# Optimization experiments

Hardware: AMD Instinct MI355X
Metric: run time of the kernel (lower is better)

Reference implementation:

```python
import jax, jax.numpy as jnp
import numpy as np

B = 16384          # batch
IN = 256           # input_dim
HID = [1024, 1024, 512]
K = 8              # num_mixtures
D = 16             # latent_dim
NT = D * (D + 1) // 2  # 136 packed tril components per mixture

_rows, _cols = np.tril_indices(D)          # row-major lower-tri order, same as nested loops
_rows = jnp.asarray(_rows); _cols = jnp.asarray(_cols)
_diag_mask = _rows == _cols                # [NT] bool


def setup_inputs() -> dict:
    key = jax.random.key(0)
    ks = jax.random.split(key, 12)

    def lin(k, fi, fo):
        kw, kb = jax.random.split(k)
        s = 1.0 / np.sqrt(fi)
        W = (jax.random.uniform(kw, (fi, fo), minval=-s, maxval=s)).astype(jnp.float32)
        b = (jax.random.uniform(kb, (fo,), minval=-s, maxval=s)).astype(jnp.float32)
        return W, b

    W0, b0 = lin(ks[0], IN, HID[0])
    W1, b1 = lin(ks[1], HID[0], HID[1])
    W2, b2 = lin(ks[2], HID[1], HID[2])
    Wpi, bpi = lin(ks[3], HID[2], K)
    Wmu, bmu = lin(ks[4], HID[2], K * D)
    Wt, bt = lin(ks[5], HID[2], K * NT)
    x = jax.random.normal(ks[6], (B, IN), dtype=jnp.float32)
    return dict(x=x, W0=W0, b0=b0, W1=W1, b1=b1, W2=W2, b2=b2,
                Wpi=Wpi, bpi=bpi, Wmu=Wmu, bmu=bmu, Wt=Wt, bt=bt)


def reference(x, W0, b0, W1, b1, W2, b2, Wpi, bpi, Wmu, bmu, Wt, bt):
    # MLP trunk: Linear + ReLU chain
    h = jax.nn.relu(x @ W0 + b0)
    h = jax.nn.relu(h @ W1 + b1)
    h = jax.nn.relu(h @ W2 + b2)
    # Heads
    pi_k = jax.nn.softmax(h @ Wpi + bpi, axis=1)                 # [B, K]
    mu_k = (h @ Wmu + bmu).reshape(-1, K, D)                     # [B, K, D]
    tc = (h @ Wt + bt).reshape(-1, K, NT)                        # [B, K, NT]
    # Fused cholesky-tril assembly: exp on diagonal entries, copy off-diagonal,
    # scattered into lower triangle in row-major (i, j<=i) order.
    vals = jnp.where(_diag_mask, jnp.exp(tc), tc)                # [B, K, NT]
    tril = jnp.zeros((tc.shape[0], K, D, D), dtype=tc.dtype)
    tril = tril.at[:, :, _rows, _cols].set(vals)                 # [B, K, D, D]
    return pi_k, mu_k, tril
```

## Files before the change

### kernel.cpp

```cpp
#include <hip/hip_runtime.h>
#include <hip/hip_bf16.h>
#include <cstdint>
#include <cstddef>

typedef __attribute__((ext_vector_type(8))) _Float16 half8;
typedef __attribute__((ext_vector_type(4))) float f32x4;
typedef __attribute__((ext_vector_type(8))) unsigned short ushort8v;
typedef __attribute__((ext_vector_type(4))) unsigned short ushort4v;

__device__ __forceinline__ unsigned short f2h_bits(float x) {
  _Float16 h = (_Float16)x;
  union { _Float16 h; unsigned short u; } cv; cv.h = h; return cv.u;
}

__device__ __forceinline__ void barrier_raw() {
  asm volatile("" ::: "memory");
  __builtin_amdgcn_s_barrier();
  asm volatile("" ::: "memory");
}
__device__ __forceinline__ void lgkm0() {
  asm volatile("s_waitcnt lgkmcnt(0)" ::: "memory");
}
template<int N> __device__ __forceinline__ void vmw() {
  static_assert(N == 0 || N == 3 || N == 4, "unsupported vmcnt");
  if constexpr (N == 0) asm volatile("s_waitcnt vmcnt(0)" ::: "memory");
  if constexpr (N == 3) asm volatile("s_waitcnt vmcnt(3)" ::: "memory");
  if constexpr (N == 4) asm volatile("s_waitcnt vmcnt(4)" ::: "memory");
}


__global__ __launch_bounds__(256) void k_f32_to_f16(const float* __restrict__ src,
                                                    unsigned short* __restrict__ dst, int n4) {
  int i = blockIdx.x * 256 + threadIdx.x;
  if (i >= n4) return;
  float4 v = ((const float4*)src)[i];
  ushort4v o;
  o[0] = f2h_bits(v.x); o[1] = f2h_bits(v.y); o[2] = f2h_bits(v.z); o[3] = f2h_bits(v.w);
  ((ushort4v*)dst)[i] = o;
}

__global__ __launch_bounds__(256) void k_transpose_f16(const float* __restrict__ W,
                                                       unsigned short* __restrict__ Wt,
                                                       int Kd, int N) {
  int tid = blockIdx.x * 256 + threadIdx.x;
  int total = (Kd >> 3) * N;
  if (tid >= total) return;
  int kc = tid / N;
  int n  = tid - kc * N;
  int k0 = kc << 3;
  ushort8v o;
#pragma unroll
  for (int j = 0; j < 8; ++j) o[j] = f2h_bits(W[(size_t)(k0 + j) * N + n]);
  *(ushort8v*)(&Wt[(size_t)n * Kd + k0]) = o;
}

__global__ __launch_bounds__(256) void k_build_head(
    const float* __restrict__ Wmu, const float* __restrict__ Wt,
    const float* __restrict__ Wpi,
    const float* __restrict__ bmu, const float* __restrict__ bt,
    const float* __restrict__ bpi,
    unsigned short* __restrict__ whd, float* __restrict__ bhd)
{
  int tid = blockIdx.x * 256 + threadIdx.x;
  if (tid >= 2304 * 64) return;
  int r  = tid >> 6;
  int d0 = (tid & 63) << 3;

  const float* src = nullptr; int stride = 0;
  if (r < 128) { src = Wmu + r; stride = 128; }
  else if (r < 2176) {
    int rU = r - 128, k = rU >> 8, i = (rU >> 4) & 15, j = rU & 15;
    if (j <= i) { src = Wt + k * 136 + ((i * (i + 1)) >> 1) + j; stride = 1088; }
  } else if (r < 2184) { src = Wpi + (r - 2176); stride = 8; }

  ushort8v o;
#pragma unroll
  for (int jj = 0; jj < 8; ++jj)
    o[jj] = src ? f2h_bits(src[(size_t)(d0 + jj) * stride]) : (unsigned short)0;
  *(ushort8v*)(&whd[(size_t)r * 512 + d0]) = o;

  if (d0 == 0) {
    float b = 0.f;
    if (r < 128) b = bmu[r];
    else if (r < 2176) {
      int rU = r - 128, k = rU >> 8, i = (rU >> 4) & 15, j = rU & 15;
      if (j <= i) b = bt[k * 136 + ((i * (i + 1)) >> 1) + j];
    } else if (r < 2184) b = bpi[r - 2176];
    bhd[r] = b;
  }
}


__device__ __forceinline__ void epi_relu_h(const f32x4& a, const float* bias, int col0,
                                           unsigned short* Hout, size_t row, int N) {
  float4 b4 = *(const float4*)&bias[col0];
  ushort4v o;
  float v0 = a[0] + b4.x; o[0] = f2h_bits(v0 > 0.f ? v0 : 0.f);
  float v1 = a[1] + b4.y; o[1] = f2h_bits(v1 > 0.f ? v1 : 0.f);
  float v2 = a[2] + b4.z; o[2] = f2h_bits(v2 > 0.f ? v2 : 0.f);
  float v3 = a[3] + b4.w; o[3] = f2h_bits(v3 > 0.f ? v3 : 0.f);
  *(ushort4v*)&Hout[row * N + col0] = o;
}

__device__ __forceinline__ void epi_head(const f32x4& a, const float* bias, int col0,
                                         size_t row, float* out_pi, float* out_mu,
                                         float* out_tril) {
  if (col0 >= 2184) return;
  float4 b4 = *(const float4*)&bias[col0];
  float v[4] = { a[0] + b4.x, a[1] + b4.y, a[2] + b4.z, a[3] + b4.w };
  if (col0 < 128) {
    *(float4*)&out_mu[row * 128 + col0] = make_float4(v[0], v[1], v[2], v[3]);
  } else if (col0 < 2176) {
    const int cc0 = col0 - 128;
    const int i   = (cc0 >> 4) & 15;
    const int j0  = cc0 & 15;
#pragma unroll
    for (int r = 0; r < 4; ++r) if (j0 + r == i) v[r] = expf(v[r]);
    *(float4*)&out_tril[row * 2048 + cc0] = make_float4(v[0], v[1], v[2], v[3]);
  } else {
    float m4 = fmaxf(fmaxf(v[0], v[1]), fmaxf(v[2], v[3]));
    float mx = fmaxf(m4, __shfl_xor(m4, 16));
    float e[4], s4 = 0.f;
#pragma unroll
    for (int r = 0; r < 4; ++r) { e[r] = expf(v[r] - mx); s4 += e[r]; }
    float sm = s4 + __shfl_xor(s4, 16);
    *(float4*)&out_pi[row * 8 + (col0 - 2176)] =
        make_float4(e[0] / sm, e[1] / sm, e[2] / sm, e[3] / sm);
  }
}


template<int EPI>
__global__ __launch_bounds__(256) void k_gemm2p(
    const unsigned short* __restrict__ A,
    const unsigned short* __restrict__ Bt,
    int Kd, int N, int nNb,
    const float* __restrict__ bias,
    unsigned short* __restrict__ Hout,
    float* __restrict__ out_pi,
    float* __restrict__ out_mu,
    float* __restrict__ out_tril)
{
  __shared__ unsigned short Alds[2][128 * 32];
  __shared__ unsigned short Blds[2][128 * 32];

  const int tid  = threadIdx.x;
  const int lane = tid & 63;
  const int wv   = tid >> 6;
  const int wr   = wv >> 1;
  const int wc   = wv & 1;
  const int l15  = lane & 15;
  const int lk   = lane >> 4;

  const int cpx = gridDim.x >> 3;
  const int bid = blockIdx.x;
  const int swz = (bid & 7) * cpx + (bid >> 3);
  const int bm  = (swz / nNb) << 7;
  const int bn  = (swz % nNb) << 7;

  f32x4 acc[4][4] = {};

  const int srow = lane >> 2;
  const int scol = (lane & 3) << 3;

  const unsigned short* aBase = A  + (size_t)bm * Kd;
  const unsigned short* bBase = Bt + (size_t)bn * Kd;

  auto stage = [&](int bb, int k0) {
#pragma unroll
    for (int c = 0; c < 2; ++c) {
      const int chunk = (wv << 1) + c;
      const int row = (chunk << 4) + srow;
      __builtin_amdgcn_global_load_lds(
          (const __attribute__((address_space(1))) void*)(aBase + (size_t)row * Kd + k0 + scol),
          (__attribute__((address_space(3))) void*)(&Alds[bb][chunk << 9]),
          16, 0, 0);
      __builtin_amdgcn_global_load_lds(
          (const __attribute__((address_space(1))) void*)(bBase + (size_t)row * Kd + k0 + scol),
          (__attribute__((address_space(3))) void*)(&Blds[bb][chunk << 9]),
          16, 0, 0);
    }
  };

  const int nk = Kd >> 5;
  stage(0, 0);
  __syncthreads();
  int cur = 0;
  for (int kt = 0; kt < nk; ++kt) {
    if (kt + 1 < nk) stage(cur ^ 1, (kt + 1) << 5);

    const unsigned short* al = &Alds[cur][((wr << 6) + l15) * 32 + (lk << 3)];
    const unsigned short* bl = &Blds[cur][((wc << 6) + l15) * 32 + (lk << 3)];
    half8 af[4], bfr[4];
#pragma unroll
    for (int m = 0; m < 4; ++m) af[m]  = *(const half8*)(al + (m << 9));
#pragma unroll
    for (int n = 0; n < 4; ++n) bfr[n] = *(const half8*)(bl + (n << 9));
#pragma unroll
    for (int m = 0; m < 4; ++m)
#pragma unroll
      for (int n = 0; n < 4; ++n)
        acc[m][n] = __builtin_amdgcn_mfma_f32_16x16x32_f16(bfr[n], af[m], acc[m][n], 0, 0, 0);

    __syncthreads();
    cur ^= 1;
  }

#pragma unroll
  for (int m = 0; m < 4; ++m) {
    const size_t row = bm + (wr << 6) + (m << 4) + l15;
#pragma unroll
    for (int n = 0; n < 4; ++n) {
      const int col0 = bn + (wc << 6) + (n << 4) + (lk << 2);
      if (EPI == 0) epi_relu_h(acc[m][n], bias, col0, Hout, row, N);
      else          epi_head(acc[m][n], bias, col0, row, out_pi, out_mu, out_tril);
    }
  }
}


template<int NH, int M_rep>
__device__ __forceinline__ void mfma_phase(const half8* af, const half8* bf,
                                           f32x4 (*acc)[4]) {
  __builtin_amdgcn_s_setprio(1);
#pragma unroll
  for (int m = 0; m < M_rep; ++m) {
    acc[m][NH * 2 + 0] = __builtin_amdgcn_mfma_f32_16x16x32_f16(bf[0], af[m], acc[m][NH * 2 + 0], 0, 0, 0);
    acc[m][NH * 2 + 1] = __builtin_amdgcn_mfma_f32_16x16x32_f16(bf[1], af[m], acc[m][NH * 2 + 1], 0, 0, 0);
  }
  __builtin_amdgcn_s_setprio(0);
}

template<int BM, int BN>
__global__ __launch_bounds__(512) void k_gemm8p(
    const unsigned short* __restrict__ A,
    const unsigned short* __restrict__ Bt,
    int Kd, int N, int nNb,
    const float* __restrict__ bias,
    unsigned short* __restrict__ Hout)
{
  constexpr int M_rep = BM / 32;
  constexpr int A_LD  = BM / 128;
  constexpr int B_LD  = BN / 128;
  constexpr int WN    = A_LD + B_LD;

  __shared__ unsigned short Ald[2][2][BM * 32];
  __shared__ unsigned short Bld[2][2][BN * 32];

  const int tid  = threadIdx.x;
  const int lane = tid & 63;
  const int wid  = tid >> 6;
  const int wm   = wid >> 2;
  const int wn   = wid & 3;
  const int l15  = lane & 15;
  const int lk   = lane >> 4;

  const int cpx = gridDim.x >> 3;
  const int bid = blockIdx.x;
  const int swz = (bid & 7) * cpx + (bid >> 3);
  const int bm  = (swz / nNb) * BM;
  const int bn  = (swz % nNb) * BN;

  const unsigned short* aBase = A  + (size_t)bm * Kd;
  const unsigned short* bBase = Bt + (size_t)bn * Kd;

  f32x4 acc[M_rep][4] = {};

  const int xo   = ((lk ^ ((l15 >> 1) & 3)) << 3);
  const int rowA = wm * (BM / 2) + l15;
  const int colB = wn * 64 + l15;

  auto stageA = [&](int bb, int h, int k0) {
#pragma unroll
    for (int i = 0; i < A_LD; ++i) {
      const int cbase = (wid << 6) + (i << 9);
      const int c_    = cbase + lane;
      const int row   = c_ >> 2;
      const int sc    = (((c_ & 3) ^ ((c_ >> 3) & 3)) << 3);
      __builtin_amdgcn_global_load_lds(
          (const __attribute__((address_space(1))) void*)(aBase + (size_t)row * Kd + k0 + h * 32 + sc),
          (__attribute__((address_space(3))) void*)(&Ald[bb][h][(size_t)cbase << 3]),
          16, 0, 0);
    }
  };
  auto stageB = [&](int bb, int h, int k0) {
#pragma unroll
    for (int i = 0; i < B_LD; ++i) {
      const int cbase = (wid << 6) + (i << 9);
      const int c_    = cbase + lane;
      const int row   = c_ >> 2;
      const int sc    = (((c_ & 3) ^ ((c_ >> 3) & 3)) << 3);
      __builtin_amdgcn_global_load_lds(
          (const __attribute__((address_space(1))) void*)(bBase + (size_t)row * Kd + k0 + h * 32 + sc),
          (__attribute__((address_space(3))) void*)(&Bld[bb][h][(size_t)cbase << 3]),
          16, 0, 0);
    }
  };

#define RD_A(kk)                                                                 \
  {                                                                              \
    _Pragma("unroll")                                                            \
    for (int m = 0; m < M_rep; ++m)                                              \
      af[m] = *(const half8*)&Ald[cur][kk][(size_t)(rowA + m * 16) * 32 + xo];   \
  }
#define RD_B(kk, nh)                                                             \
  {                                                                              \
    _Pragma("unroll")                                                            \
    for (int n2 = 0; n2 < 2; ++n2)                                               \
      bf[n2] = *(const half8*)&Bld[cur][kk][(size_t)(colB + ((nh) * 2 + n2) * 16) * 32 + xo]; \
  }

  const int nk = Kd >> 6;
  stageA(0, 0, 0); stageB(0, 0, 0); stageA(0, 1, 0); stageB(0, 1, 0);
  vmw<WN>();
  barrier_raw();

  int cur = 0;
  for (int kt = 0; kt < nk; ++kt) {
    const bool pre = (kt + 1 < nk);
    const int  k0n = (kt + 1) << 6;
    half8 af[M_rep], bf[2];

    RD_A(0); RD_B(0, 0);
    if (pre) stageA(cur ^ 1, 0, k0n);
    barrier_raw(); lgkm0();
    mfma_phase<0, M_rep>(af, bf, acc);
    barrier_raw();

    RD_B(0, 1);
    if (pre) stageB(cur ^ 1, 0, k0n);
    barrier_raw(); lgkm0();
    mfma_phase<1, M_rep>(af, bf, acc);
    if (pre) vmw<WN>(); else vmw<0>();
    barrier_raw();

    RD_A(1); RD_B(1, 0);
    if (pre) stageA(cur ^ 1, 1, k0n);
    barrier_raw(); lgkm0();
    mfma_phase<0, M_rep>(af, bf, acc);
    barrier_raw();

    RD_B(1, 1);
    if (pre) stageB(cur ^ 1, 1, k0n);
    barrier_raw(); lgkm0();
    mfma_phase<1, M_rep>(af, bf, acc);
    if (pre) vmw<WN>();
    barrier_raw();

    cur ^= 1;
  }
#undef RD_A
#undef RD_B

#pragma unroll
  for (int m = 0; m < M_rep; ++m) {
    const size_t row = bm + wm * (BM / 2) + (m << 4) + l15;
#pragma unroll
    for (int n = 0; n < 4; ++n) {
      const int col0 = bn + wn * 64 + (n << 4) + (lk << 2);
      epi_relu_h(acc[m][n], bias, col0, Hout, row, N);
    }
  }
}


extern "C" void kernel_launch(void* const* d_in, const int* in_sizes, int n_in,
                              void* d_out, int out_size, void* d_ws, size_t ws_size,
                              hipStream_t stream)
{
  const float* x   = (const float*)d_in[0];
  const float* W0  = (const float*)d_in[1];
  const float* b0  = (const float*)d_in[2];
  const float* W1  = (const float*)d_in[3];
  const float* b1  = (const float*)d_in[4];
  const float* W2  = (const float*)d_in[5];
  const float* b2  = (const float*)d_in[6];
  const float* Wpi = (const float*)d_in[7];
  const float* bpi = (const float*)d_in[8];
  const float* Wmu = (const float*)d_in[9];
  const float* bmu = (const float*)d_in[10];
  const float* Wt  = (const float*)d_in[11];
  const float* bt  = (const float*)d_in[12];

  char* ws = (char*)d_ws;
  unsigned short* xh  = (unsigned short*)(ws);
  unsigned short* h0  = (unsigned short*)(ws + 8388608);
  unsigned short* h1  = (unsigned short*)(ws + 41943040);
  unsigned short* h2  = (unsigned short*)(ws + 8388608);
  unsigned short* w0b = (unsigned short*)(ws + 75497472);
  unsigned short* w1b = (unsigned short*)(ws + 76021760);
  unsigned short* w2b = (unsigned short*)(ws + 78118912);
  unsigned short* whd = (unsigned short*)(ws + 79167488);
  float*          bhd = (float*)         (ws + 81526784);

  float* out_pi   = (float*)d_out;
  float* out_mu   = (float*)d_out + 131072;
  float* out_tril = (float*)d_out + 2228224;

  k_f32_to_f16<<<4096, 256, 0, stream>>>(x, xh, 1048576);
  k_transpose_f16<<<128, 256, 0, stream>>>(W0, w0b, 256, 1024);
  k_transpose_f16<<<512, 256, 0, stream>>>(W1, w1b, 1024, 1024);
  k_transpose_f16<<<256, 256, 0, stream>>>(W2, w2b, 1024, 512);
  k_build_head<<<576, 256, 0, stream>>>(Wmu, Wt, Wpi, bmu, bt, bpi, whd, bhd);

  k_gemm2p<0><<<1024, 256, 0, stream>>>(xh, w0b, 256, 1024, 8, b0, h0,
                                        nullptr, nullptr, nullptr);
  k_gemm8p<256, 256><<<256, 512, 0, stream>>>(h0, w1b, 1024, 1024, 4, b1, h1);
  k_gemm8p<128, 256><<<256, 512, 0, stream>>>(h1, w2b, 1024, 512, 2, b2, h2);
  k_gemm2p<1><<<2304, 256, 0, stream>>>(h2, whd, 512, 2304, 18, bhd, nullptr,
                                        out_pi, out_mu, out_tril);
}
```

Baseline: 185.6 us.

## Triple-buffer LDS in small GEMMs with XOR swizzle and vmcnt-based waits

Converts the 128x128 GEMM used for the first layer and the fused head from double to triple LDS buffering. It prefetches two k-tiles ahead and waits with explicit vmcnt counts instead of __syncthreads. It XOR-swizzles the LDS column layout to reduce bank conflicts on fragment reads, and raises wave priority around the MFMA block. The cost is more LDS per block, which may lower occupancy, plus fragile hand-tuned wait counts.

```diff
diff --git a/kernel.cpp b/kernel.cpp
--- a/kernel.cpp
+++ b/kernel.cpp
@@ -17,15 +17,15 @@
   asm volatile("" ::: "memory");
   __builtin_amdgcn_s_barrier();
   asm volatile("" ::: "memory");
-}
-__device__ __forceinline__ void lgkm0() {
-  asm volatile("s_waitcnt lgkmcnt(0)" ::: "memory");
 }
 template<int N> __device__ __forceinline__ void vmw() {
   static_assert(N == 0 || N == 3 || N == 4, "unsupported vmcnt");
   if constexpr (N == 0) asm volatile("s_waitcnt vmcnt(0)" ::: "memory");
   if constexpr (N == 3) asm volatile("s_waitcnt vmcnt(3)" ::: "memory");
   if constexpr (N == 4) asm volatile("s_waitcnt vmcnt(4)" ::: "memory");
+}
+__device__ __forceinline__ void lgkm0() {
+  asm volatile("s_waitcnt lgkmcnt(0)" ::: "memory");
 }
 
 
@@ -131,7 +131,7 @@
 
 
 template<int EPI>
-__global__ __launch_bounds__(256) void k_gemm2p(
+__global__ __launch_bounds__(256) void k_gemm3b(
     const unsigned short* __restrict__ A,
     const unsigned short* __restrict__ Bt,
     int Kd, int N, int nNb,
@@ -141,8 +141,8 @@
     float* __restrict__ out_mu,
     float* __restrict__ out_tril)
 {
-  __shared__ unsigned short Alds[2][128 * 32];
-  __shared__ unsigned short Blds[2][128 * 32];
+  __shared__ unsigned short Ald[3][128 * 32];
+  __shared__ unsigned short Bld[3][128 * 32];
 
   const int tid  = threadIdx.x;
   const int lane = tid & 63;
@@ -160,50 +160,62 @@
 
   f32x4 acc[4][4] = {};
 
-  const int srow = lane >> 2;
-  const int scol = (lane & 3) << 3;
-
   const unsigned short* aBase = A  + (size_t)bm * Kd;
   const unsigned short* bBase = Bt + (size_t)bn * Kd;
 
-  auto stage = [&](int bb, int k0) {
-#pragma unroll
-    for (int c = 0; c < 2; ++c) {
-      const int chunk = (wv << 1) + c;
-      const int row = (chunk << 4) + srow;
+  const int xo = ((lk ^ ((l15 >> 1) & 3)) << 3);
+
+  auto stage = [&](int bb, int kt) {
+    const int k0 = kt << 5;
+#pragma unroll
+    for (int i = 0; i < 2; ++i) {
+      const int cbase = (wv << 6) + (i << 8);
+      const int c_    = cbase + lane;
+      const int row   = c_ >> 2;
+      const int sc    = (((c_ & 3) ^ ((c_ >> 3) & 3)) << 3);
       __builtin_amdgcn_global_load_lds(
-          (const __attribute__((address_space(1))) void*)(aBase + (size_t)row * Kd + k0 + scol),
-          (__attribute__((address_space(3))) void*)(&Alds[bb][chunk << 9]),
+          (const __attribute__((address_space(1))) void*)(aBase + (size_t)row * Kd + k0 + sc),
+          (__attribute__((address_space(3))) void*)(&Ald[bb][cbase << 3]),
           16, 0, 0);
       __builtin_amdgcn_global_load_lds(
-          (const __attribute__((address_space(1))) void*)(bBase + (size_t)row * Kd + k0 + scol),
-          (__attribute__((address_space(3))) void*)(&Blds[bb][chunk << 9]),
+          (const __attribute__((address_space(1))) void*)(bBase + (size_t)row * Kd + k0 + sc),
+          (__attribute__((address_space(3))) void*)(&Bld[bb][cbase << 3]),
           16, 0, 0);
     }
   };
 
   const int nk = Kd >> 5;
   stage(0, 0);
-  __syncthreads();
-  int cur = 0;
+  stage(1, 1);
+  vmw<4>();
+  barrier_raw();
+
+  int i0 = 0, i1 = 1, i2 = 2;
   for (int kt = 0; kt < nk; ++kt) {
-    if (kt + 1 < nk) stage(cur ^ 1, (kt + 1) << 5);
-
-    const unsigned short* al = &Alds[cur][((wr << 6) + l15) * 32 + (lk << 3)];
-    const unsigned short* bl = &Blds[cur][((wc << 6) + l15) * 32 + (lk << 3)];
+    if (kt + 2 < nk) stage(i2, kt + 2);
+
     half8 af[4], bfr[4];
 #pragma unroll
-    for (int m = 0; m < 4; ++m) af[m]  = *(const half8*)(al + (m << 9));
-#pragma unroll
-    for (int n = 0; n < 4; ++n) bfr[n] = *(const half8*)(bl + (n << 9));
+    for (int m = 0; m < 4; ++m)
+      af[m]  = *(const half8*)&Ald[i0][((wr << 6) + (m << 4) + l15) * 32 + xo];
+#pragma unroll
+    for (int n = 0; n < 4; ++n)
+      bfr[n] = *(const half8*)&Bld[i0][((wc << 6) + (n << 4) + l15) * 32 + xo];
+
+    __builtin_amdgcn_s_setprio(1);
 #pragma unroll
     for (int m = 0; m < 4; ++m)
 #pragma unroll
       for (int n = 0; n < 4; ++n)
         acc[m][n] = __builtin_amdgcn_mfma_f32_16x16x32_f16(bfr[n], af[m], acc[m][n], 0, 0, 0);
-
-    __syncthreads();
-    cur ^= 1;
+    __builtin_amdgcn_s_setprio(0);
+
+    if (kt + 1 < nk) {
+      if (kt + 2 < nk) vmw<4>();
+      else             vmw<0>();
+      barrier_raw();
+    }
+    const int t = i0; i0 = i1; i1 = i2; i2 = t;
   }
 
 #pragma unroll
@@ -403,10 +415,10 @@
   k_transpose_f16<<<256, 256, 0, stream>>>(W2, w2b, 1024, 512);
   k_build_head<<<576, 256, 0, stream>>>(Wmu, Wt, Wpi, bmu, bt, bpi, whd, bhd);
 
-  k_gemm2p<0><<<1024, 256, 0, stream>>>(xh, w0b, 256, 1024, 8, b0, h0,
+  k_gemm3b<0><<<1024, 256, 0, stream>>>(xh, w0b, 256, 1024, 8, b0, h0,
                                         nullptr, nullptr, nullptr);
   k_gemm8p<256, 256><<<256, 512, 0, stream>>>(h0, w1b, 1024, 1024, 4, b1, h1);
   k_gemm8p<128, 256><<<256, 512, 0, stream>>>(h1, w2b, 1024, 512, 2, b2, h2);
-  k_gemm2p<1><<<2304, 256, 0, stream>>>(h2, whd, 512, 2304, 18, bhd, nullptr,
+  k_gemm3b<1><<<2304, 256, 0, stream>>>(h2, whd, 512, 2304, 18, bhd, nullptr,
                                         out_pi, out_mu, out_tril);
 }
```

Result: no change. 185.9 us (+0.2%).
